# Kernel optimization log

Hardware: AMD Instinct MI355X
Metric: run time of the kernel (lower is better)

## Reference

```python
import jax, jax.numpy as jnp
import numpy as np


def setup_inputs() -> dict:
    key = jax.random.key(0)
    k1, k2 = jax.random.split(key)
    B, L = 8192, 4096
    v = jax.random.normal(k1, (B, L), dtype=jnp.float32)
    z = jax.random.normal(k2, (B, L), dtype=jnp.float32)
    return {"v": v, "z": z}


def reference(v, z):
    # Householder reflection: z_new = z - 2 * v (v . z) / ||v||^2
    # Mathematically identical to the original bmm(v v^T, z) formulation,
    # but contracts the rank-1 outer product analytically (no BxLxL tensor).
    vz = jnp.sum(v * z, axis=1, keepdims=True)        # [B, 1] = v . z per row
    norm_sq = jnp.sum(v * v, axis=1, keepdims=True)    # [B, 1] = ||v||^2
    return z - 2.0 * v * (vz / norm_sq)
```

## Files before the change

kernel.cpp:

```cpp
#include <hip/hip_runtime.h>


#define L_DIM 4096
#define BLOCK 512
#define VEC (L_DIM / 4)
#define PER_THREAD (VEC / BLOCK)
#define NWAVES (BLOCK / 64)

typedef float f4 __attribute__((ext_vector_type(4)));

__global__ __launch_bounds__(BLOCK) void householder_kernel(
    const float* __restrict__ v,
    const float* __restrict__ z,
    float* __restrict__ out,
    int B)
{
    __shared__ float s_red[2][NWAVES];

    const int row = blockIdx.x;
    if (row >= B) return;
    const size_t base = (size_t)row * L_DIM;
    const f4* v4 = (const f4*)(v + base);
    const f4* z4 = (const f4*)(z + base);
    f4* o4 = (f4*)(out + base);

    f4 a[PER_THREAD], b[PER_THREAD];
    #pragma unroll
    for (int k = 0; k < PER_THREAD; ++k) {
        const int i = threadIdx.x + k * BLOCK;
        a[k] = v4[i];
        b[k] = z4[i];
    }

    float vz = 0.0f, vv = 0.0f;
    #pragma unroll
    for (int k = 0; k < PER_THREAD; ++k) {
        vz = fmaf(a[k].x, b[k].x, vz); vz = fmaf(a[k].y, b[k].y, vz);
        vz = fmaf(a[k].z, b[k].z, vz); vz = fmaf(a[k].w, b[k].w, vz);
        vv = fmaf(a[k].x, a[k].x, vv); vv = fmaf(a[k].y, a[k].y, vv);
        vv = fmaf(a[k].z, a[k].z, vv); vv = fmaf(a[k].w, a[k].w, vv);
    }

    #pragma unroll
    for (int off = 32; off > 0; off >>= 1) {
        vz += __shfl_down(vz, off, 64);
        vv += __shfl_down(vv, off, 64);
    }

    const int wave = threadIdx.x >> 6;
    if ((threadIdx.x & 63) == 0) {
        s_red[0][wave] = vz;
        s_red[1][wave] = vv;
    }
    __syncthreads();

    float tvz = 0.0f, tvv = 0.0f;
    #pragma unroll
    for (int w = 0; w < NWAVES; ++w) {
        tvz += s_red[0][w];
        tvv += s_red[1][w];
    }
    const float s = -2.0f * tvz / tvv;

    #pragma unroll
    for (int k = 0; k < PER_THREAD; ++k) {
        const int i = threadIdx.x + k * BLOCK;
        f4 r;
        r.x = fmaf(s, a[k].x, b[k].x);
        r.y = fmaf(s, a[k].y, b[k].y);
        r.z = fmaf(s, a[k].z, b[k].z);
        r.w = fmaf(s, a[k].w, b[k].w);
        __builtin_nontemporal_store(r, &o4[i]);
    }
}

extern "C" void kernel_launch(void* const* d_in, const int* in_sizes, int n_in,
                              void* d_out, int out_size, void* d_ws, size_t ws_size,
                              hipStream_t stream) {
    const float* v = (const float*)d_in[0];
    const float* z = (const float*)d_in[1];
    float* out = (float*)d_out;
    const int B = in_sizes[0] / L_DIM;
    householder_kernel<<<B, BLOCK, 0, stream>>>(v, z, out, B);
}
```

Measured before the change: 313.5 us.

## Use persistent blocks with double-buffered row prefetch in registers

Replaces one-block-per-row with a persistent grid capped at 2048 blocks of 256 threads. Each block loops over rows and prefetches the next row's v and z into a second register set while reducing and writing the current row. Stores switch from nontemporal to plain. This hides load latency across rows and amortizes launch overhead, at the cost of doubled register use (lower occupancy) and a parity-indexed shared reduction buffer.

```diff
diff --git a/kernel.cpp b/kernel.cpp
--- a/kernel.cpp
+++ b/kernel.cpp
@@ -2,43 +2,41 @@
 
 
 #define L_DIM 4096
-#define BLOCK 512
+#define BLOCK 256
 #define VEC (L_DIM / 4)
 #define PER_THREAD (VEC / BLOCK)
 #define NWAVES (BLOCK / 64)
 
 typedef float f4 __attribute__((ext_vector_type(4)));
 
-__global__ __launch_bounds__(BLOCK) void householder_kernel(
-    const float* __restrict__ v,
-    const float* __restrict__ z,
-    float* __restrict__ out,
-    int B)
+__device__ __forceinline__ void load_row(
+    const float* __restrict__ v, const float* __restrict__ z,
+    size_t row, int tid,
+    f4 (&A)[PER_THREAD], f4 (&Bv)[PER_THREAD])
 {
-    __shared__ float s_red[2][NWAVES];
-
-    const int row = blockIdx.x;
-    if (row >= B) return;
-    const size_t base = (size_t)row * L_DIM;
-    const f4* v4 = (const f4*)(v + base);
-    const f4* z4 = (const f4*)(z + base);
-    f4* o4 = (f4*)(out + base);
-
-    f4 a[PER_THREAD], b[PER_THREAD];
+    const f4* v4 = (const f4*)(v + row * L_DIM);
+    const f4* z4 = (const f4*)(z + row * L_DIM);
     #pragma unroll
     for (int k = 0; k < PER_THREAD; ++k) {
-        const int i = threadIdx.x + k * BLOCK;
-        a[k] = v4[i];
-        b[k] = z4[i];
+        const int i = tid + k * BLOCK;
+        A[k]  = v4[i];
+        Bv[k] = z4[i];
     }
+}
 
+template <int PAR>
+__device__ __forceinline__ void process_row(
+    float* __restrict__ out, size_t row, int tid,
+    const f4 (&A)[PER_THREAD], const f4 (&Bv)[PER_THREAD],
+    float (&s_red)[2][2][NWAVES])
+{
     float vz = 0.0f, vv = 0.0f;
     #pragma unroll
     for (int k = 0; k < PER_THREAD; ++k) {
-        vz = fmaf(a[k].x, b[k].x, vz); vz = fmaf(a[k].y, b[k].y, vz);
-        vz = fmaf(a[k].z, b[k].z, vz); vz = fmaf(a[k].w, b[k].w, vz);
-        vv = fmaf(a[k].x, a[k].x, vv); vv = fmaf(a[k].y, a[k].y, vv);
-        vv = fmaf(a[k].z, a[k].z, vv); vv = fmaf(a[k].w, a[k].w, vv);
+        vz = fmaf(A[k].x, Bv[k].x, vz); vz = fmaf(A[k].y, Bv[k].y, vz);
+        vz = fmaf(A[k].z, Bv[k].z, vz); vz = fmaf(A[k].w, Bv[k].w, vz);
+        vv = fmaf(A[k].x, A[k].x, vv);  vv = fmaf(A[k].y, A[k].y, vv);
+        vv = fmaf(A[k].z, A[k].z, vv);  vv = fmaf(A[k].w, A[k].w, vv);
     }
 
     #pragma unroll
@@ -47,30 +45,61 @@
         vv += __shfl_down(vv, off, 64);
     }
 
-    const int wave = threadIdx.x >> 6;
-    if ((threadIdx.x & 63) == 0) {
-        s_red[0][wave] = vz;
-        s_red[1][wave] = vv;
+    const int wave = tid >> 6;
+    if ((tid & 63) == 0) {
+        s_red[PAR][0][wave] = vz;
+        s_red[PAR][1][wave] = vv;
     }
     __syncthreads();
 
     float tvz = 0.0f, tvv = 0.0f;
     #pragma unroll
     for (int w = 0; w < NWAVES; ++w) {
-        tvz += s_red[0][w];
-        tvv += s_red[1][w];
+        tvz += s_red[PAR][0][w];
+        tvv += s_red[PAR][1][w];
     }
     const float s = -2.0f * tvz / tvv;
 
+    f4* o4 = (f4*)(out + row * L_DIM);
     #pragma unroll
     for (int k = 0; k < PER_THREAD; ++k) {
-        const int i = threadIdx.x + k * BLOCK;
+        const int i = tid + k * BLOCK;
         f4 r;
-        r.x = fmaf(s, a[k].x, b[k].x);
-        r.y = fmaf(s, a[k].y, b[k].y);
-        r.z = fmaf(s, a[k].z, b[k].z);
-        r.w = fmaf(s, a[k].w, b[k].w);
-        __builtin_nontemporal_store(r, &o4[i]);
+        r.x = fmaf(s, A[k].x, Bv[k].x);
+        r.y = fmaf(s, A[k].y, Bv[k].y);
+        r.z = fmaf(s, A[k].z, Bv[k].z);
+        r.w = fmaf(s, A[k].w, Bv[k].w);
+        o4[i] = r;
+    }
+}
+
+__global__ __launch_bounds__(BLOCK) void householder_kernel(
+    const float* __restrict__ v,
+    const float* __restrict__ z,
+    float* __restrict__ out,
+    int B)
+{
+    __shared__ float s_red[2][2][NWAVES];
+
+    const int tid = threadIdx.x;
+    const int g = gridDim.x;
+    int r = blockIdx.x;
+    if (r >= B) return;
+
+    f4 a0[PER_THREAD], b0[PER_THREAD], a1[PER_THREAD], b1[PER_THREAD];
+    load_row(v, z, (size_t)r, tid, a0, b0);
+
+    for (;;) {
+        const int r1 = r + g;
+        if (r1 < B) load_row(v, z, (size_t)r1, tid, a1, b1);
+        process_row<0>(out, (size_t)r, tid, a0, b0, s_red);
+        if (r1 >= B) return;
+
+        const int r2 = r1 + g;
+        if (r2 < B) load_row(v, z, (size_t)r2, tid, a0, b0);
+        process_row<1>(out, (size_t)r1, tid, a1, b1, s_red);
+        if (r2 >= B) return;
+        r = r2;
     }
 }
 
@@ -81,5 +110,6 @@
     const float* z = (const float*)d_in[1];
     float* out = (float*)d_out;
     const int B = in_sizes[0] / L_DIM;
-    householder_kernel<<<B, BLOCK, 0, stream>>>(v, z, out, B);
+    const int grid = (B < 2048) ? B : 2048;
+    householder_kernel<<<grid, BLOCK, 0, stream>>>(v, z, out, B);
 }
```

New measurement: 308.7 us. About the same (-1.6%).

## Assign one wavefront per row and drop block-level shared-memory reduction

Applied to the files above, without the earlier changes.

Each 64-lane wave now processes a whole row, holding 16 float4 of v and z per lane in registers, with 4 rows per 256-thread block. The cross-wave shared-memory reduction and __syncthreads are replaced by an xor-shuffle butterfly, and partial sums use four independent accumulators to shorten dependency chains. Output stores switch from nontemporal to regular stores. The cost is much higher register usage per thread and therefore lower occupancy.

```diff
diff --git a/kernel.cpp b/kernel.cpp
--- a/kernel.cpp
+++ b/kernel.cpp
@@ -2,75 +2,77 @@
 
 
 #define L_DIM 4096
-#define BLOCK 512
-#define VEC (L_DIM / 4)
-#define PER_THREAD (VEC / BLOCK)
-#define NWAVES (BLOCK / 64)
+#define BLOCK 256
+#define WPB (BLOCK / 64)
+#define NF4 (L_DIM / 4 / 64)
 
 typedef float f4 __attribute__((ext_vector_type(4)));
 
-__global__ __launch_bounds__(BLOCK) void householder_kernel(
+__global__ __launch_bounds__(BLOCK, 3) void householder_kernel(
     const float* __restrict__ v,
     const float* __restrict__ z,
     float* __restrict__ out,
     int B)
 {
-    __shared__ float s_red[2][NWAVES];
+    const int wave = threadIdx.x >> 6;
+    const int lane = threadIdx.x & 63;
+    const int row = blockIdx.x * WPB + wave;
+    if (row >= B) return;
 
-    const int row = blockIdx.x;
-    if (row >= B) return;
     const size_t base = (size_t)row * L_DIM;
     const f4* v4 = (const f4*)(v + base);
     const f4* z4 = (const f4*)(z + base);
     f4* o4 = (f4*)(out + base);
 
-    f4 a[PER_THREAD], b[PER_THREAD];
+    f4 a[NF4], b[NF4];
     #pragma unroll
-    for (int k = 0; k < PER_THREAD; ++k) {
-        const int i = threadIdx.x + k * BLOCK;
-        a[k] = v4[i];
-        b[k] = z4[i];
+    for (int j = 0; j < NF4; ++j) {
+        a[j] = v4[lane + j * 64];
+        b[j] = z4[lane + j * 64];
     }
 
-    float vz = 0.0f, vv = 0.0f;
+    float vz0 = 0.f, vz1 = 0.f, vz2 = 0.f, vz3 = 0.f;
+    float vv0 = 0.f, vv1 = 0.f, vv2 = 0.f, vv3 = 0.f;
     #pragma unroll
-    for (int k = 0; k < PER_THREAD; ++k) {
-        vz = fmaf(a[k].x, b[k].x, vz); vz = fmaf(a[k].y, b[k].y, vz);
-        vz = fmaf(a[k].z, b[k].z, vz); vz = fmaf(a[k].w, b[k].w, vz);
-        vv = fmaf(a[k].x, a[k].x, vv); vv = fmaf(a[k].y, a[k].y, vv);
-        vv = fmaf(a[k].z, a[k].z, vv); vv = fmaf(a[k].w, a[k].w, vv);
+    for (int j = 0; j < NF4; j += 4) {
+        vz0 = fmaf(a[j+0].x, b[j+0].x, vz0); vz0 = fmaf(a[j+0].y, b[j+0].y, vz0);
+        vz0 = fmaf(a[j+0].z, b[j+0].z, vz0); vz0 = fmaf(a[j+0].w, b[j+0].w, vz0);
+        vv0 = fmaf(a[j+0].x, a[j+0].x, vv0); vv0 = fmaf(a[j+0].y, a[j+0].y, vv0);
+        vv0 = fmaf(a[j+0].z, a[j+0].z, vv0); vv0 = fmaf(a[j+0].w, a[j+0].w, vv0);
+
+        vz1 = fmaf(a[j+1].x, b[j+1].x, vz1); vz1 = fmaf(a[j+1].y, b[j+1].y, vz1);
+        vz1 = fmaf(a[j+1].z, b[j+1].z, vz1); vz1 = fmaf(a[j+1].w, b[j+1].w, vz1);
+        vv1 = fmaf(a[j+1].x, a[j+1].x, vv1); vv1 = fmaf(a[j+1].y, a[j+1].y, vv1);
+        vv1 = fmaf(a[j+1].z, a[j+1].z, vv1); vv1 = fmaf(a[j+1].w, a[j+1].w, vv1);
+
+        vz2 = fmaf(a[j+2].x, b[j+2].x, vz2); vz2 = fmaf(a[j+2].y, b[j+2].y, vz2);
+        vz2 = fmaf(a[j+2].z, b[j+2].z, vz2); vz2 = fmaf(a[j+2].w, b[j+2].w, vz2);
+        vv2 = fmaf(a[j+2].x, a[j+2].x, vv2); vv2 = fmaf(a[j+2].y, a[j+2].y, vv2);
+        vv2 = fmaf(a[j+2].z, a[j+2].z, vv2); vv2 = fmaf(a[j+2].w, a[j+2].w, vv2);
+
+        vz3 = fmaf(a[j+3].x, b[j+3].x, vz3); vz3 = fmaf(a[j+3].y, b[j+3].y, vz3);
+        vz3 = fmaf(a[j+3].z, b[j+3].z, vz3); vz3 = fmaf(a[j+3].w, b[j+3].w, vz3);
+        vv3 = fmaf(a[j+3].x, a[j+3].x, vv3); vv3 = fmaf(a[j+3].y, a[j+3].y, vv3);
+        vv3 = fmaf(a[j+3].w, a[j+3].w, vv3); vv3 = fmaf(a[j+3].z, a[j+3].z, vv3);
     }
+    float vz = (vz0 + vz1) + (vz2 + vz3);
+    float vv = (vv0 + vv1) + (vv2 + vv3);
 
     #pragma unroll
     for (int off = 32; off > 0; off >>= 1) {
-        vz += __shfl_down(vz, off, 64);
-        vv += __shfl_down(vv, off, 64);
+        vz += __shfl_xor(vz, off, 64);
+        vv += __shfl_xor(vv, off, 64);
     }
-
-    const int wave = threadIdx.x >> 6;
-    if ((threadIdx.x & 63) == 0) {
-        s_red[0][wave] = vz;
-        s_red[1][wave] = vv;
-    }
-    __syncthreads();
-
-    float tvz = 0.0f, tvv = 0.0f;
-    #pragma unroll
-    for (int w = 0; w < NWAVES; ++w) {
-        tvz += s_red[0][w];
-        tvv += s_red[1][w];
-    }
-    const float s = -2.0f * tvz / tvv;
+    const float s = -2.0f * vz / vv;
 
     #pragma unroll
-    for (int k = 0; k < PER_THREAD; ++k) {
-        const int i = threadIdx.x + k * BLOCK;
+    for (int j = 0; j < NF4; ++j) {
         f4 r;
-        r.x = fmaf(s, a[k].x, b[k].x);
-        r.y = fmaf(s, a[k].y, b[k].y);
-        r.z = fmaf(s, a[k].z, b[k].z);
-        r.w = fmaf(s, a[k].w, b[k].w);
-        __builtin_nontemporal_store(r, &o4[i]);
+        r.x = fmaf(s, a[j].x, b[j].x);
+        r.y = fmaf(s, a[j].y, b[j].y);
+        r.z = fmaf(s, a[j].z, b[j].z);
+        r.w = fmaf(s, a[j].w, b[j].w);
+        o4[lane + j * 64] = r;
     }
 }
 
@@ -81,5 +83,6 @@
     const float* z = (const float*)d_in[1];
     float* out = (float*)d_out;
     const int B = in_sizes[0] / L_DIM;
-    householder_kernel<<<B, BLOCK, 0, stream>>>(v, z, out, B);
+    const int grid = (B + WPB - 1) / WPB;
+    householder_kernel<<<grid, BLOCK, 0, stream>>>(v, z, out, B);
 }
```

Result: no change. 311.1 us (-0.8%).
